# Optimization experiments

Hardware: AMD Instinct MI355X
Metric: run time of the kernel (lower is better)

Reference implementation:

```python
import jax, jax.numpy as jnp
import numpy as np

B, SRC_LEN, IN_DIM = 4096, 128, 16
H = 64
SEQ_LEN = 100
MEAN_DIM = 4
COV_DIM = MEAN_DIM + MEAN_DIM * (MEAN_DIM - 1) // 2  # 10
SKIP = 4


def _lin_init(key, out_d, in_d):
    k1, k2 = jax.random.split(key)
    bound = 1.0 / np.sqrt(in_d)
    W = jax.random.uniform(k1, (out_d, in_d), minval=-bound, maxval=bound, dtype=jnp.float32)
    b = jax.random.uniform(k2, (out_d,), minval=-bound, maxval=bound, dtype=jnp.float32)
    return W, b


def setup_inputs() -> dict:
    key = jax.random.key(0)
    ks = jax.random.split(key, 16)
    inp = {}
    inp["x"] = jax.random.normal(ks[0], (B, SRC_LEN, IN_DIM), dtype=jnp.float32)
    inp["trg"] = jax.random.normal(ks[1], (B, 1, SKIP), dtype=jnp.float32)
    # encoder GRU (1 layer)
    inp["enc_Wih"], inp["enc_bih"] = _lin_init(ks[2], 3 * H, IN_DIM)
    inp["enc_Whh"], inp["enc_bhh"] = _lin_init(ks[3], 3 * H, H)
    # decoder GRU (1 layer)
    inp["dec_Wih"], inp["dec_bih"] = _lin_init(ks[4], 3 * H, IN_DIM)
    inp["dec_Whh"], inp["dec_bhh"] = _lin_init(ks[5], 3 * H, H)
    # decoder.out: Linear(H -> IN_DIM)
    inp["out_W"], inp["out_b"] = _lin_init(ks[6], IN_DIM, H)
    # initEmbed: Linear(SKIP -> IN_DIM)
    inp["emb_W"], inp["emb_b"] = _lin_init(ks[7], IN_DIM, SKIP)
    # mean head: Linear(IN_DIM->H), GELU, Linear(H->MEAN_DIM)
    inp["mh_W1"], inp["mh_b1"] = _lin_init(ks[8], H, IN_DIM)
    inp["mh_W2"], inp["mh_b2"] = _lin_init(ks[9], MEAN_DIM, H)
    # cov head: Linear(IN_DIM->H), GELU, Linear(H->COV_DIM)
    inp["ch_W1"], inp["ch_b1"] = _lin_init(ks[10], H, IN_DIM)
    inp["ch_W2"], inp["ch_b2"] = _lin_init(ks[11], COV_DIM, H)
    return inp


def _gru_cell(h, xt, Wih, Whh, bih, bhh):
    # PyTorch GRU cell math. h, xt: [B, H], [B, in]
    gi = xt @ Wih.T + bih           # [B, 3H]
    gh = h @ Whh.T + bhh            # [B, 3H]
    i_r, i_z, i_n = jnp.split(gi, 3, axis=-1)
    h_r, h_z, h_n = jnp.split(gh, 3, axis=-1)
    r = jax.nn.sigmoid(i_r + h_r)
    z = jax.nn.sigmoid(i_z + h_z)
    n = jnp.tanh(i_n + r * h_n)
    return (1.0 - z) * n + z * h


def reference(x, trg, enc_Wih, enc_bih, enc_Whh, enc_bhh,
              dec_Wih, dec_bih, dec_Whh, dec_bhh,
              out_W, out_b, emb_W, emb_b,
              mh_W1, mh_b1, mh_W2, mh_b2,
              ch_W1, ch_b1, ch_W2, ch_b2):
    b = x.shape[0]
    # ---- encoder GRU over src_len; only final hidden is used downstream ----
    h0 = jnp.zeros((b, H), dtype=x.dtype)

    def enc_step(h, xt):
        h = _gru_cell(h, xt, enc_Wih, enc_Whh, enc_bih, enc_bhh)
        return h, None

    enc_h, _ = jax.lax.scan(enc_step, h0, jnp.swapaxes(x, 0, 1))

    init_in = trg[:, 0, :] @ emb_W.T + emb_b  # [B, IN_DIM]

    def dec_step(carry, _):
        h, inp = carry
        h = _gru_cell(h, inp, dec_Wih, dec_Whh, dec_bih, dec_bhh)
        o = h @ out_W.T + out_b               # [B, IN_DIM]
        nxt = jax.lax.stop_gradient(o)        # .detach() on fed-back input
        return (h, nxt), o

    (_, _), outs = jax.lax.scan(dec_step, (enc_h, init_in), None, length=SEQ_LEN)
    dec_out = jnp.swapaxes(outs, 0, 1)        # [B, SEQ_LEN, IN_DIM]

    # ---- output heads (Dropout is identity in eval) ----
    means = jax.nn.gelu(dec_out @ mh_W1.T + mh_b1, approximate=False) @ mh_W2.T + mh_b2
    covs = jax.nn.gelu(dec_out @ ch_W1.T + ch_b1, approximate=False) @ ch_W2.T + ch_b2

    inf = jnp.inf
    lower = jnp.array([-inf, -inf, -1.0, -1.0], dtype=means.dtype)
    upper = jnp.array([inf, inf, 1.0, 1.0], dtype=means.dtype)
    means = jnp.maximum(jnp.minimum(means, upper), lower)
    return means, covs
```

## Files before the change

kernel.cpp:

```cpp
#include <hip/hip_runtime.h>
#include <cstdint>
#include <cstddef>

#define BTOT    4096
#define SRCLEN  128
#define INDIM   16
#define HDIM    64
#define SEQLEN  100
#define MEANS_N (BTOT * SEQLEN * 4)

__device__ __forceinline__ float sigmoidf_(float x) {
    return __builtin_amdgcn_rcpf(1.0f + __expf(-x));
}
__device__ __forceinline__ float tanhf_(float x) {
    float e = __expf(2.0f * x);
    return 1.0f - 2.0f * __builtin_amdgcn_rcpf(e + 1.0f);
}
__device__ __forceinline__ float gelu_fast(float x) {
    float z = fabsf(x) * 0.70710678118654752440f;
    float t = __builtin_amdgcn_rcpf(1.0f + 0.3275911f * z);
    float p = t * (0.254829592f +
              t * (-0.284496736f +
              t * (1.421413741f +
              t * (-1.453152027f +
              t * 1.061405429f))));
    float er = 1.0f - p * __expf(-z * z);
    er = copysignf(er, x);
    return 0.5f * x * (1.0f + er);
}

typedef __attribute__((ext_vector_type(8))) short s8v;
typedef __attribute__((ext_vector_type(4))) float f4v;

__device__ __forceinline__ unsigned short f2bf(float x) {
    unsigned u = __float_as_uint(x);
    unsigned r = (u + 0x7FFFu + ((u >> 16) & 1u)) >> 16;
    return (unsigned short)r;
}
__device__ __forceinline__ float bf2f(unsigned short b) {
    return __uint_as_float(((unsigned)b) << 16);
}
__device__ __forceinline__ void split2(float4 a, float4 b, s8v& hi, s8v& lo) {
    float v[8] = {a.x, a.y, a.z, a.w, b.x, b.y, b.z, b.w};
    #pragma unroll
    for (int j = 0; j < 8; ++j) {
        unsigned short h = f2bf(v[j]);
        hi[j] = (short)h;
        lo[j] = (short)f2bf(v[j] - bf2f(h));
    }
}
__device__ __forceinline__ void split8(const float* v, s8v& hi, s8v& lo) {
    #pragma unroll
    for (int j = 0; j < 8; ++j) {
        unsigned short h = f2bf(v[j]);
        hi[j] = (short)h;
        lo[j] = (short)f2bf(v[j] - bf2f(h));
    }
}
__device__ __forceinline__ void load_bfrag(const float* p, s8v& hi, s8v& lo) {
    float4 a = *(const float4*)p;
    float4 b = *(const float4*)(p + 4);
    split2(a, b, hi, lo);
}

typedef __attribute__((ext_vector_type(2))) unsigned int u2v;
__device__ __forceinline__ float half_merge(float own_lo, float send_hi) {
    u2v r = __builtin_amdgcn_permlane32_swap(__float_as_uint(own_lo),
                                             __float_as_uint(send_hi),
                                             false, false);
    return __uint_as_float(r[0]);
}

#define MFMA16(a, b, c) __builtin_amdgcn_mfma_f32_16x16x32_bf16((a), (b), (c), 0, 0, 0)

__global__ __launch_bounds__(256, 2) void enc_mfma_kernel(
    const float* __restrict__ x,
    const float* __restrict__ Wih, const float* __restrict__ bih,
    const float* __restrict__ Whh, const float* __restrict__ bhh,
    float* __restrict__ enc_h)
{
    const int tid  = threadIdx.x;
    const int lane = tid & 63;
    const int w    = tid >> 6;
    const int col  = lane & 15;
    const int q    = lane >> 4;
    const int u    = w * 16 + col;
    const int b0   = blockIdx.x * 8;
    const int rj0  = (q & 1) * 4 + ((q >> 1) << 1);

    __shared__ __align__(16) unsigned short hiL[2][16][72];
    __shared__ __align__(16) unsigned short loL[2][16][72];
    __shared__ __align__(16) unsigned short xhi_l[64][9][16];
    __shared__ __align__(16) unsigned short xlo_l[64][9][16];

    for (int i = tid; i < 2 * 16 * 72; i += 256) {
        ((unsigned short*)hiL)[i] = 0;
        ((unsigned short*)loL)[i] = 0;
    }
    for (int i = tid; i < 64 * 16; i += 256) {
        xhi_l[i >> 4][8][i & 15] = 0;
        xlo_l[i >> 4][8][i & 15] = 0;
    }

    auto stage_x = [&](int c) {
        #pragma unroll
        for (int k = 0; k < 8; ++k) {
            int f   = tid + k * 256;
            int b   = f >> 8;
            int rem = f & 255;
            int tl  = rem >> 2;
            int d4  = (rem & 3) << 2;
            const float* xp = x + ((size_t)(b0 + b) * SRCLEN + (c * 64 + tl)) * INDIM + d4;
            float4 v = *(const float4*)xp;
            float vv[4] = {v.x, v.y, v.z, v.w};
            unsigned short hh[4], ll[4];
            #pragma unroll
            for (int j = 0; j < 4; ++j) {
                hh[j] = f2bf(vv[j]);
                ll[j] = f2bf(vv[j] - bf2f(hh[j]));
            }
            *(ushort4*)&xhi_l[tl][b][d4] = make_ushort4(hh[0], hh[1], hh[2], hh[3]);
            *(ushort4*)&xlo_l[tl][b][d4] = make_ushort4(ll[0], ll[1], ll[2], ll[3]);
        }
    };

    const s8v z8 = {0, 0, 0, 0, 0, 0, 0, 0};
    const f4v z4 = {0.0f, 0.0f, 0.0f, 0.0f};

    s8v brh[3], brl[3], bzh[3], bzl[3], bnhh[2], bnhl[2], bnxh, bnxl;
    load_bfrag(Whh + (size_t)u * 64 + q * 8,              brh[0], brl[0]);
    load_bfrag(Whh + (size_t)u * 64 + 32 + q * 8,         brh[1], brl[1]);
    load_bfrag(Whh + (size_t)(64 + u) * 64 + q * 8,       bzh[0], bzl[0]);
    load_bfrag(Whh + (size_t)(64 + u) * 64 + 32 + q * 8,  bzh[1], bzl[1]);
    load_bfrag(Whh + (size_t)(128 + u) * 64 + q * 8,      bnhh[0], bnhl[0]);
    load_bfrag(Whh + (size_t)(128 + u) * 64 + 32 + q * 8, bnhh[1], bnhl[1]);
    if (q < 2) {
        load_bfrag(Wih + (size_t)u * 16 + q * 8,         brh[2], brl[2]);
        load_bfrag(Wih + (size_t)(64 + u) * 16 + q * 8,  bzh[2], bzl[2]);
        load_bfrag(Wih + (size_t)(128 + u) * 16 + q * 8, bnxh, bnxl);
    } else {
        brh[2] = z8; brl[2] = z8; bzh[2] = z8; bzl[2] = z8; bnxh = z8; bnxl = z8;
    }

    const float br   = bih[u] + bhh[u];
    const float bz   = bih[u + 64] + bhh[u + 64];
    const float bnx  = bih[u + 128];
    const float bnh  = bhh[u + 128];

    const int xb   = (q < 2) ? (col & 7) : 8;
    const int xoff = (q & 1) * 8;
    const unsigned short* xh_base = &xhi_l[0][xb][xoff];
    const unsigned short* xl_base = &xlo_l[0][xb][xoff];

    stage_x(0);
    float hold2[2] = {0.0f, 0.0f};
    __syncthreads();

    int cur = 0;
    for (int t = 0; t < SRCLEN; ++t) {
        if (t == 64) {
            stage_x(1);
            __syncthreads();
        }
        const int tl = t & 63;

        const s8v xh = *(const s8v*)(xh_base + (size_t)tl * 144);
        const s8v xl = *(const s8v*)(xl_base + (size_t)tl * 144);

        const s8v ah0 = *(const s8v*)&hiL[cur][col][q * 8];
        const s8v al0 = *(const s8v*)&loL[cur][col][q * 8];
        const s8v ah1 = *(const s8v*)&hiL[cur][col][32 + q * 8];
        const s8v al1 = *(const s8v*)&loL[cur][col][32 + q * 8];

        f4v accr, accz, accnh, accnx;
        accr  = MFMA16(ah0, brh[0], z4);
        accz  = MFMA16(ah0, bzh[0], z4);
        accnh = MFMA16(ah0, bnhh[0], z4);
        accr  = MFMA16(ah0, brl[0], accr);
        accz  = MFMA16(ah0, bzl[0], accz);
        accnh = MFMA16(ah0, bnhl[0], accnh);
        accr  = MFMA16(al0, brh[0], accr);
        accz  = MFMA16(al0, bzh[0], accz);
        accnh = MFMA16(al0, bnhh[0], accnh);
        accr  = MFMA16(ah1, brh[1], accr);
        accz  = MFMA16(ah1, bzh[1], accz);
        accnh = MFMA16(ah1, bnhh[1], accnh);
        accr  = MFMA16(ah1, brl[1], accr);
        accz  = MFMA16(ah1, bzl[1], accz);
        accnh = MFMA16(ah1, bnhl[1], accnh);
        accr  = MFMA16(al1, brh[1], accr);
        accz  = MFMA16(al1, bzh[1], accz);
        accnh = MFMA16(al1, bnhh[1], accnh);
        accr  = MFMA16(xh, brh[2], accr);
        accz  = MFMA16(xh, bzh[2], accz);
        accnx = MFMA16(xh, bnxh, z4);
        accr  = MFMA16(xh, brl[2], accr);
        accz  = MFMA16(xh, bzl[2], accz);
        accnx = MFMA16(xh, bnxl, accnx);
        accr  = MFMA16(xl, brh[2], accr);
        accz  = MFMA16(xl, bzh[2], accz);
        accnx = MFMA16(xl, bnxh, accnx);

        float pr[2], pz[2], pnh[2], pnx[2];
        pr[0]  = half_merge(accr[0],  accr[2]);
        pr[1]  = half_merge(accr[1],  accr[3]);
        pz[0]  = half_merge(accz[0],  accz[2]);
        pz[1]  = half_merge(accz[1],  accz[3]);
        pnh[0] = half_merge(accnh[0], accnh[2]);
        pnh[1] = half_merge(accnh[1], accnh[3]);
        pnx[0] = half_merge(accnx[0], accnx[2]);
        pnx[1] = half_merge(accnx[1], accnx[3]);

        const int nxt = cur ^ 1;
        #pragma unroll
        for (int j = 0; j < 2; ++j) {
            float r  = sigmoidf_(pr[j] + br);
            float zz = sigmoidf_(pz[j] + bz);
            float n  = tanhf_(pnx[j] + bnx + r * (pnh[j] + bnh));
            float h  = (1.0f - zz) * n + zz * hold2[j];
            hold2[j] = h;
            unsigned short hh = f2bf(h);
            hiL[nxt][rj0 + j][u] = hh;
            loL[nxt][rj0 + j][u] = f2bf(h - bf2f(hh));
        }
        __syncthreads();
        cur ^= 1;
    }

    enc_h[(size_t)(b0 + rj0) * HDIM + u]     = hold2[0];
    enc_h[(size_t)(b0 + rj0 + 1) * HDIM + u] = hold2[1];
}

__global__ __launch_bounds__(256, 2) void dec_mfma_kernel(
    const float* __restrict__ trg,
    const float* __restrict__ Wih, const float* __restrict__ bih,
    const float* __restrict__ Whh, const float* __restrict__ bhh,
    const float* __restrict__ outW, const float* __restrict__ outb,
    const float* __restrict__ embW, const float* __restrict__ embb,
    const float* __restrict__ enc_h,
    float* __restrict__ dec_o)
{
    const int tid  = threadIdx.x;
    const int lane = tid & 63;
    const int w    = tid >> 6;
    const int col  = lane & 15;
    const int q    = lane >> 4;
    const int u    = w * 16 + col;
    const int b0   = blockIdx.x * 8;
    const int rj0  = (q & 1) * 4 + ((q >> 1) << 1);

    __shared__ __align__(16) unsigned short hiL[2][16][72];
    __shared__ __align__(16) unsigned short loL[2][16][72];
    __shared__ float outW_l[16][64];
    __shared__ float init_l[8][16];

    for (int i = tid; i < 16 * 64; i += 256) outW_l[i >> 6][i & 63] = outW[i];
    if (tid < 128) {
        int b = tid >> 4, jj = tid & 15;
        float s = embb[jj];
        #pragma unroll
        for (int s4 = 0; s4 < 4; ++s4)
            s = fmaf(embW[jj * 4 + s4], trg[(size_t)(b0 + b) * 4 + s4], s);
        init_l[b][jj] = s;
    }
    for (int i = tid; i < 2 * 8 * 72; i += 256) {
        int buf = i / (8 * 72);
        int rr  = (i / 72) & 7;
        int cc  = i % 72;
        hiL[buf][8 + rr][cc] = 0;
        loL[buf][8 + rr][cc] = 0;
    }
    if (tid < 128) {
        int idx = tid * 4;
        int bb = idx >> 6, uu = idx & 63;
        float4 v = *(const float4*)(enc_h + (size_t)(b0 + bb) * HDIM + uu);
        float vv[4] = {v.x, v.y, v.z, v.w};
        #pragma unroll
        for (int j = 0; j < 4; ++j) {
            unsigned short hh = f2bf(vv[j]);
            hiL[0][bb][uu + j] = hh;
            loL[0][bb][uu + j] = f2bf(vv[j] - bf2f(hh));
        }
    }
    float hold2[2];
    hold2[0] = enc_h[(size_t)(b0 + rj0) * HDIM + u];
    hold2[1] = enc_h[(size_t)(b0 + rj0 + 1) * HDIM + u];

    __syncthreads();

    const f4v z4 = {0.0f, 0.0f, 0.0f, 0.0f};

    float wh_r[16], wh_z[16], wh_n[16];
    #pragma unroll
    for (int c = 0; c < 2; ++c)
        #pragma unroll
        for (int jj = 0; jj < 8; ++jj) {
            int k = c * 32 + q * 8 + jj;
            wh_r[c * 8 + jj] = Whh[(size_t)u * 64 + k];
            wh_z[c * 8 + jj] = Whh[(size_t)(64 + u) * 64 + k];
            wh_n[c * 8 + jj] = Whh[(size_t)(128 + u) * 64 + k];
        }
    float wi_r[16], wi_z[16], wi_n[16];
    #pragma unroll
    for (int j = 0; j < 16; ++j) {
        wi_r[j] = Wih[(size_t)u * 16 + j];
        wi_z[j] = Wih[(size_t)(64 + u) * 16 + j];
        wi_n[j] = Wih[(size_t)(128 + u) * 16 + j];
    }

    float m_r[16], m_z[16], c_in[16];
    #pragma unroll
    for (int c = 0; c < 2; ++c)
        #pragma unroll
        for (int jj = 0; jj < 8; ++jj) {
            int k = c * 32 + q * 8 + jj;
            float sr = 0.0f, sz = 0.0f, sn = 0.0f;
            #pragma unroll
            for (int j = 0; j < 16; ++j) {
                float ow = outW_l[j][k];
                sr = fmaf(wi_r[j], ow, sr);
                sz = fmaf(wi_z[j], ow, sz);
                sn = fmaf(wi_n[j], ow, sn);
            }
            m_r[c * 8 + jj]  = wh_r[c * 8 + jj] + sr;
            m_z[c * 8 + jj]  = wh_z[c * 8 + jj] + sz;
            c_in[c * 8 + jj] = sn;
        }

    s8v mrh[2], mrl[2], mzh[2], mzl[2], cinh[2], cinl[2], hnh[2], hnl[2];
    split8(m_r,      mrh[0],  mrl[0]);  split8(m_r + 8,  mrh[1],  mrl[1]);
    split8(m_z,      mzh[0],  mzl[0]);  split8(m_z + 8,  mzh[1],  mzl[1]);
    split8(c_in,     cinh[0], cinl[0]); split8(c_in + 8, cinh[1], cinl[1]);
    split8(wh_n,     hnh[0],  hnl[0]);  split8(wh_n + 8, hnh[1],  hnl[1]);
    s8v r0h[2], r0l[2], z0h[2], z0l[2];
    split8(wh_r, r0h[0], r0l[0]); split8(wh_r + 8, r0h[1], r0l[1]);
    split8(wh_z, z0h[0], z0l[0]); split8(wh_z + 8, z0h[1], z0l[1]);
    s8v owh[2], owl[2];
    {
        float ov[16];
        #pragma unroll
        for (int c = 0; c < 2; ++c)
            #pragma unroll
            for (int jj = 0; jj < 8; ++jj)
                ov[c * 8 + jj] = outW_l[col][c * 32 + q * 8 + jj];
        split8(ov, owh[0], owl[0]); split8(ov + 8, owh[1], owl[1]);
    }

    float b_r = bhh[u] + bih[u];
    float b_z = bhh[u + 64] + bih[u + 64];
    float b_in = bih[u + 128];
    const float b_hn = bhh[u + 128];
    #pragma unroll
    for (int j = 0; j < 16; ++j) {
        float obj = outb[j];
        b_r  = fmaf(obj, wi_r[j], b_r);
        b_z  = fmaf(obj, wi_z[j], b_z);
        b_in = fmaf(obj, wi_n[j], b_in);
    }
    const float ob = outb[col];

    float g_r[2], g_z[2], g_n[2];
    #pragma unroll
    for (int j2 = 0; j2 < 2; ++j2) {
        int row = rj0 + j2;
        float sr = bih[u] + bhh[u];
        float sz = bih[u + 64] + bhh[u + 64];
        float sn = bih[u + 128];
        #pragma unroll
        for (int j = 0; j < 16; ++j) {
            float iv = init_l[row][j];
            sr = fmaf(wi_r[j], iv, sr);
            sz = fmaf(wi_z[j], iv, sz);
            sn = fmaf(wi_n[j], iv, sn);
        }
        g_r[j2] = sr; g_z[j2] = sz; g_n[j2] = sn;
    }

    {
        const s8v ah0 = *(const s8v*)&hiL[0][col][q * 8];
        const s8v al0 = *(const s8v*)&loL[0][col][q * 8];
        const s8v ah1 = *(const s8v*)&hiL[0][col][32 + q * 8];
        const s8v al1 = *(const s8v*)&loL[0][col][32 + q * 8];
        f4v ar, az, ahn;
        ar  = MFMA16(ah0, r0h[0], z4);
        az  = MFMA16(ah0, z0h[0], z4);
        ahn = MFMA16(ah0, hnh[0], z4);
        ar  = MFMA16(ah0, r0l[0], ar);
        az  = MFMA16(ah0, z0l[0], az);
        ahn = MFMA16(ah0, hnl[0], ahn);
        ar  = MFMA16(al0, r0h[0], ar);
        az  = MFMA16(al0, z0h[0], az);
        ahn = MFMA16(al0, hnh[0], ahn);
        ar  = MFMA16(ah1, r0h[1], ar);
        az  = MFMA16(ah1, z0h[1], az);
        ahn = MFMA16(ah1, hnh[1], ahn);
        ar  = MFMA16(ah1, r0l[1], ar);
        az  = MFMA16(ah1, z0l[1], az);
        ahn = MFMA16(ah1, hnl[1], ahn);
        ar  = MFMA16(al1, r0h[1], ar);
        az  = MFMA16(al1, z0h[1], az);
        ahn = MFMA16(al1, hnh[1], ahn);

        float pr[2], pz[2], pnh[2];
        pr[0]  = half_merge(ar[0],  ar[2]);
        pr[1]  = half_merge(ar[1],  ar[3]);
        pz[0]  = half_merge(az[0],  az[2]);
        pz[1]  = half_merge(az[1],  az[3]);
        pnh[0] = half_merge(ahn[0], ahn[2]);
        pnh[1] = half_merge(ahn[1], ahn[3]);

        #pragma unroll
        for (int j = 0; j < 2; ++j) {
            float r  = sigmoidf_(pr[j] + g_r[j]);
            float zz = sigmoidf_(pz[j] + g_z[j]);
            float n  = tanhf_(g_n[j] + r * (pnh[j] + b_hn));
            float h  = (1.0f - zz) * n + zz * hold2[j];
            hold2[j] = h;
            unsigned short hh = f2bf(h);
            hiL[1][rj0 + j][u] = hh;
            loL[1][rj0 + j][u] = f2bf(h - bf2f(hh));
        }
        __syncthreads();
    }

    for (int t = 1; t < SEQLEN; ++t) {
        const int cur = t & 1;
        const s8v ah0 = *(const s8v*)&hiL[cur][col][q * 8];
        const s8v al0 = *(const s8v*)&loL[cur][col][q * 8];
        const s8v ah1 = *(const s8v*)&hiL[cur][col][32 + q * 8];
        const s8v al1 = *(const s8v*)&loL[cur][col][32 + q * 8];

        if (w == ((t - 1) & 3)) {
            f4v oa;
            oa = MFMA16(ah0, owh[0], z4);
            oa = MFMA16(ah0, owl[0], oa);
            oa = MFMA16(al0, owh[0], oa);
            oa = MFMA16(ah1, owh[1], oa);
            oa = MFMA16(ah1, owl[1], oa);
            oa = MFMA16(al1, owh[1], oa);
            if (q < 2) {
                #pragma unroll
                for (int i = 0; i < 4; ++i)
                    dec_o[(((size_t)(b0 + q * 4 + i) * SEQLEN) + (t - 1)) * INDIM + col] = oa[i] + ob;
            }
        }

        f4v ar, az, ain, ahn;
        ar  = MFMA16(ah0, mrh[0], z4);
        az  = MFMA16(ah0, mzh[0], z4);
        ain = MFMA16(ah0, cinh[0], z4);
        ahn = MFMA16(ah0, hnh[0], z4);
        ar  = MFMA16(ah0, mrl[0], ar);
        az  = MFMA16(ah0, mzl[0], az);
        ain = MFMA16(ah0, cinl[0], ain);
        ahn = MFMA16(ah0, hnl[0], ahn);
        ar  = MFMA16(al0, mrh[0], ar);
        az  = MFMA16(al0, mzh[0], az);
        ain = MFMA16(al0, cinh[0], ain);
        ahn = MFMA16(al0, hnh[0], ahn);
        ar  = MFMA16(ah1, mrh[1], ar);
        az  = MFMA16(ah1, mzh[1], az);
        ain = MFMA16(ah1, cinh[1], ain);
        ahn = MFMA16(ah1, hnh[1], ahn);
        ar  = MFMA16(ah1, mrl[1], ar);
        az  = MFMA16(ah1, mzl[1], az);
        ain = MFMA16(ah1, cinl[1], ain);
        ahn = MFMA16(ah1, hnl[1], ahn);
        ar  = MFMA16(al1, mrh[1], ar);
        az  = MFMA16(al1, mzh[1], az);
        ain = MFMA16(al1, cinh[1], ain);
        ahn = MFMA16(al1, hnh[1], ahn);

        float pr[2], pz[2], pin[2], pnh[2];
        pr[0]  = half_merge(ar[0],  ar[2]);
        pr[1]  = half_merge(ar[1],  ar[3]);
        pz[0]  = half_merge(az[0],  az[2]);
        pz[1]  = half_merge(az[1],  az[3]);
        pin[0] = half_merge(ain[0], ain[2]);
        pin[1] = half_merge(ain[1], ain[3]);
        pnh[0] = half_merge(ahn[0], ahn[2]);
        pnh[1] = half_merge(ahn[1], ahn[3]);

        const int nxt = cur ^ 1;
        #pragma unroll
        for (int j = 0; j < 2; ++j) {
            float r  = sigmoidf_(pr[j] + b_r);
            float zz = sigmoidf_(pz[j] + b_z);
            float n  = tanhf_(pin[j] + b_in + r * (pnh[j] + b_hn));
            float h  = (1.0f - zz) * n + zz * hold2[j];
            hold2[j] = h;
            unsigned short hh = f2bf(h);
            hiL[nxt][rj0 + j][u] = hh;
            loL[nxt][rj0 + j][u] = f2bf(h - bf2f(hh));
        }
        __syncthreads();
    }

    if (w == 0) {
        const s8v ah0 = *(const s8v*)&hiL[0][col][q * 8];
        const s8v al0 = *(const s8v*)&loL[0][col][q * 8];
        const s8v ah1 = *(const s8v*)&hiL[0][col][32 + q * 8];
        const s8v al1 = *(const s8v*)&loL[0][col][32 + q * 8];
        f4v oa;
        oa = MFMA16(ah0, owh[0], z4);
        oa = MFMA16(ah0, owl[0], oa);
        oa = MFMA16(al0, owh[0], oa);
        oa = MFMA16(ah1, owh[1], oa);
        oa = MFMA16(ah1, owl[1], oa);
        oa = MFMA16(al1, owh[1], oa);
        if (q < 2) {
            #pragma unroll
            for (int i = 0; i < 4; ++i)
                dec_o[(((size_t)(b0 + q * 4 + i) * SEQLEN) + (SEQLEN - 1)) * INDIM + col] = oa[i] + ob;
        }
    }
}

__global__ __launch_bounds__(256) void heads_kernel(
    const float* __restrict__ dec_o,
    const float* __restrict__ mW1, const float* __restrict__ mb1,
    const float* __restrict__ mW2, const float* __restrict__ mb2,
    const float* __restrict__ cW1, const float* __restrict__ cb1,
    const float* __restrict__ cW2, const float* __restrict__ cb2,
    float* __restrict__ out)
{
    const int tid = threadIdx.x;

    __shared__ __align__(16) float lW1m[64][16];
    __shared__ __align__(16) float lW1c[64][16];
    __shared__ __align__(16) float lW2t[64][16];

    for (int i = tid; i < 1024; i += 256) {
        lW1m[i >> 4][i & 15] = mW1[i];
        lW1c[i >> 4][i & 15] = cW1[i];
    }
    if (tid < 64) {
        #pragma unroll
        for (int j = 0; j < 4; ++j)  lW2t[tid][j]     = mW2[j * 64 + tid];
        #pragma unroll
        for (int j = 0; j < 10; ++j) lW2t[tid][4 + j] = cW2[j * 64 + tid];
        lW2t[tid][14] = mb1[tid];
        lW2t[tid][15] = cb1[tid];
    }
    __syncthreads();

    const size_t r = (size_t)blockIdx.x * 256 + tid;

    float o16[16];
    {
        const float4* op = (const float4*)(dec_o + r * 16);
        #pragma unroll
        for (int c = 0; c < 4; ++c) {
            float4 v = op[c];
            o16[4 * c + 0] = v.x; o16[4 * c + 1] = v.y;
            o16[4 * c + 2] = v.z; o16[4 * c + 3] = v.w;
        }
    }

    float m[4], cv[10];
    #pragma unroll
    for (int j = 0; j < 4; ++j)  m[j]  = mb2[j];
    #pragma unroll
    for (int j = 0; j < 10; ++j) cv[j] = cb2[j];

    #pragma unroll 4
    for (int hu = 0; hu < 64; ++hu) {
        const float4 a0 = *(const float4*)&lW1m[hu][0];
        const float4 a1 = *(const float4*)&lW1m[hu][4];
        const float4 a2 = *(const float4*)&lW1m[hu][8];
        const float4 a3 = *(const float4*)&lW1m[hu][12];
        const float4 c0 = *(const float4*)&lW1c[hu][0];
        const float4 c1 = *(const float4*)&lW1c[hu][4];
        const float4 c2 = *(const float4*)&lW1c[hu][8];
        const float4 c3 = *(const float4*)&lW1c[hu][12];
        const float4 t0 = *(const float4*)&lW2t[hu][0];
        const float4 t1 = *(const float4*)&lW2t[hu][4];
        const float4 t2 = *(const float4*)&lW2t[hu][8];
        const float4 t3 = *(const float4*)&lW2t[hu][12];

        float hm = t3.z;
        hm = fmaf(a0.x, o16[0],  hm); hm = fmaf(a0.y, o16[1],  hm);
        hm = fmaf(a0.z, o16[2],  hm); hm = fmaf(a0.w, o16[3],  hm);
        hm = fmaf(a1.x, o16[4],  hm); hm = fmaf(a1.y, o16[5],  hm);
        hm = fmaf(a1.z, o16[6],  hm); hm = fmaf(a1.w, o16[7],  hm);
        hm = fmaf(a2.x, o16[8],  hm); hm = fmaf(a2.y, o16[9],  hm);
        hm = fmaf(a2.z, o16[10], hm); hm = fmaf(a2.w, o16[11], hm);
        hm = fmaf(a3.x, o16[12], hm); hm = fmaf(a3.y, o16[13], hm);
        hm = fmaf(a3.z, o16[14], hm); hm = fmaf(a3.w, o16[15], hm);
        float gm = gelu_fast(hm);
        m[0] = fmaf(t0.x, gm, m[0]); m[1] = fmaf(t0.y, gm, m[1]);
        m[2] = fmaf(t0.z, gm, m[2]); m[3] = fmaf(t0.w, gm, m[3]);

        float hc = t3.w;
        hc = fmaf(c0.x, o16[0],  hc); hc = fmaf(c0.y, o16[1],  hc);
        hc = fmaf(c0.z, o16[2],  hc); hc = fmaf(c0.w, o16[3],  hc);
        hc = fmaf(c1.x, o16[4],  hc); hc = fmaf(c1.y, o16[5],  hc);
        hc = fmaf(c1.z, o16[6],  hc); hc = fmaf(c1.w, o16[7],  hc);
        hc = fmaf(c2.x, o16[8],  hc); hc = fmaf(c2.y, o16[9],  hc);
        hc = fmaf(c2.z, o16[10], hc); hc = fmaf(c2.w, o16[11], hc);
        hc = fmaf(c3.x, o16[12], hc); hc = fmaf(c3.y, o16[13], hc);
        hc = fmaf(c3.z, o16[14], hc); hc = fmaf(c3.w, o16[15], hc);
        float gc = gelu_fast(hc);
        cv[0] = fmaf(t1.x, gc, cv[0]); cv[1] = fmaf(t1.y, gc, cv[1]);
        cv[2] = fmaf(t1.z, gc, cv[2]); cv[3] = fmaf(t1.w, gc, cv[3]);
        cv[4] = fmaf(t2.x, gc, cv[4]); cv[5] = fmaf(t2.y, gc, cv[5]);
        cv[6] = fmaf(t2.z, gc, cv[6]); cv[7] = fmaf(t2.w, gc, cv[7]);
        cv[8] = fmaf(t3.x, gc, cv[8]); cv[9] = fmaf(t3.y, gc, cv[9]);
    }

    m[2] = fminf(fmaxf(m[2], -1.0f), 1.0f);
    m[3] = fminf(fmaxf(m[3], -1.0f), 1.0f);

    float* means = out;
    float* covs  = out + MEANS_N;
    #pragma unroll
    for (int j = 0; j < 4; ++j)  means[r * 4 + j]  = m[j];
    #pragma unroll
    for (int j = 0; j < 10; ++j) covs[r * 10 + j]  = cv[j];
}

extern "C" void kernel_launch(void* const* d_in, const int* in_sizes, int n_in,
                              void* d_out, int out_size, void* d_ws, size_t ws_size,
                              hipStream_t stream)
{
    const float* x    = (const float*)d_in[0];
    const float* trg  = (const float*)d_in[1];
    const float* eWih = (const float*)d_in[2];
    const float* ebih = (const float*)d_in[3];
    const float* eWhh = (const float*)d_in[4];
    const float* ebhh = (const float*)d_in[5];
    const float* dWih = (const float*)d_in[6];
    const float* dbih = (const float*)d_in[7];
    const float* dWhh = (const float*)d_in[8];
    const float* dbhh = (const float*)d_in[9];
    const float* outW = (const float*)d_in[10];
    const float* outb = (const float*)d_in[11];
    const float* embW = (const float*)d_in[12];
    const float* embb = (const float*)d_in[13];
    const float* mW1  = (const float*)d_in[14];
    const float* mb1  = (const float*)d_in[15];
    const float* mW2  = (const float*)d_in[16];
    const float* mb2  = (const float*)d_in[17];
    const float* cW1  = (const float*)d_in[18];
    const float* cb1  = (const float*)d_in[19];
    const float* cW2  = (const float*)d_in[20];
    const float* cb2  = (const float*)d_in[21];

    float* ws    = (float*)d_ws;
    float* enc_h = ws;
    float* dec_o = ws + (size_t)BTOT * HDIM;
    float* outp  = (float*)d_out;

    enc_mfma_kernel<<<dim3(BTOT / 8), dim3(256), 0, stream>>>(x, eWih, ebih, eWhh, ebhh, enc_h);
    dec_mfma_kernel<<<dim3(BTOT / 8), dim3(256), 0, stream>>>(trg, dWih, dbih, dWhh, dbhh,
                                                              outW, outb, embW, embb, enc_h, dec_o);
    heads_kernel<<<dim3((BTOT * SEQLEN) / 256), dim3(256), 0, stream>>>(
        dec_o, mW1, mb1, mW2, mb2, cW1, cb1, cW2, cb2, outp);
}
```

Before: 347.9 us.

## Split encoder GRU gates across two wave groups with 16 batches per block

The encoder kernel now uses 512 threads and 16 batch rows per block, filling the full 16-row MFMA tile instead of half of it. Four waves compute the r gate and the recurrent n term, and the other four compute the z gate and the input n term, exchanging partial results through shared memory. The aim is to halve the blocks and MFMA work per batch row and to shorten each wave's serial MFMA chain per time step. The cost is an extra __syncthreads per step, an LDS round trip for the exchanged gates, and more frequent x staging in 32-step chunks.

```diff
diff --git a/kernel.cpp b/kernel.cpp
--- a/kernel.cpp
+++ b/kernel.cpp
@@ -73,7 +73,7 @@
 
 #define MFMA16(a, b, c) __builtin_amdgcn_mfma_f32_16x16x32_bf16((a), (b), (c), 0, 0, 0)
 
-__global__ __launch_bounds__(256, 2) void enc_mfma_kernel(
+__global__ __launch_bounds__(512, 2) void enc_mfma_kernel(
     const float* __restrict__ x,
     const float* __restrict__ Wih, const float* __restrict__ bih,
     const float* __restrict__ Whh, const float* __restrict__ bhh,
@@ -82,35 +82,37 @@
     const int tid  = threadIdx.x;
     const int lane = tid & 63;
     const int w    = tid >> 6;
+    const int p    = w & 3;
+    const bool isA = (w < 4);
     const int col  = lane & 15;
     const int q    = lane >> 4;
-    const int u    = w * 16 + col;
-    const int b0   = blockIdx.x * 8;
-    const int rj0  = (q & 1) * 4 + ((q >> 1) << 1);
+    const int u    = p * 16 + col;
+    const int b0   = blockIdx.x * 16;
 
     __shared__ __align__(16) unsigned short hiL[2][16][72];
     __shared__ __align__(16) unsigned short loL[2][16][72];
-    __shared__ __align__(16) unsigned short xhi_l[64][9][16];
-    __shared__ __align__(16) unsigned short xlo_l[64][9][16];
-
-    for (int i = tid; i < 2 * 16 * 72; i += 256) {
+    __shared__ __align__(16) unsigned short xhi_l[32][17][16];
+    __shared__ __align__(16) unsigned short xlo_l[32][17][16];
+    __shared__ float zx_l[4][8][64];
+
+    for (int i = tid; i < 2 * 16 * 72; i += 512) {
         ((unsigned short*)hiL)[i] = 0;
         ((unsigned short*)loL)[i] = 0;
     }
-    for (int i = tid; i < 64 * 16; i += 256) {
-        xhi_l[i >> 4][8][i & 15] = 0;
-        xlo_l[i >> 4][8][i & 15] = 0;
+    for (int i = tid; i < 32 * 16; i += 512) {
+        xhi_l[i >> 4][16][i & 15] = 0;
+        xlo_l[i >> 4][16][i & 15] = 0;
     }
 
     auto stage_x = [&](int c) {
         #pragma unroll
-        for (int k = 0; k < 8; ++k) {
-            int f   = tid + k * 256;
-            int b   = f >> 8;
-            int rem = f & 255;
+        for (int k = 0; k < 4; ++k) {
+            int f   = tid + k * 512;
+            int b   = f >> 7;
+            int rem = f & 127;
             int tl  = rem >> 2;
             int d4  = (rem & 3) << 2;
-            const float* xp = x + ((size_t)(b0 + b) * SRCLEN + (c * 64 + tl)) * INDIM + d4;
+            const float* xp = x + ((size_t)(b0 + b) * SRCLEN + (c * 32 + tl)) * INDIM + d4;
             float4 v = *(const float4*)xp;
             float vv[4] = {v.x, v.y, v.z, v.w};
             unsigned short hh[4], ll[4];
@@ -127,108 +129,107 @@
     const s8v z8 = {0, 0, 0, 0, 0, 0, 0, 0};
     const f4v z4 = {0.0f, 0.0f, 0.0f, 0.0f};
 
-    s8v brh[3], brl[3], bzh[3], bzl[3], bnhh[2], bnhl[2], bnxh, bnxl;
-    load_bfrag(Whh + (size_t)u * 64 + q * 8,              brh[0], brl[0]);
-    load_bfrag(Whh + (size_t)u * 64 + 32 + q * 8,         brh[1], brl[1]);
-    load_bfrag(Whh + (size_t)(64 + u) * 64 + q * 8,       bzh[0], bzl[0]);
-    load_bfrag(Whh + (size_t)(64 + u) * 64 + 32 + q * 8,  bzh[1], bzl[1]);
-    load_bfrag(Whh + (size_t)(128 + u) * 64 + q * 8,      bnhh[0], bnhl[0]);
-    load_bfrag(Whh + (size_t)(128 + u) * 64 + 32 + q * 8, bnhh[1], bnhl[1]);
-    if (q < 2) {
-        load_bfrag(Wih + (size_t)u * 16 + q * 8,         brh[2], brl[2]);
-        load_bfrag(Wih + (size_t)(64 + u) * 16 + q * 8,  bzh[2], bzl[2]);
-        load_bfrag(Wih + (size_t)(128 + u) * 16 + q * 8, bnxh, bnxl);
+    const int g1row = (isA ? 0 : 64) + u;
+    s8v g1h[3], g1l[3];
+    s8v g2h[2], g2l[2];
+    load_bfrag(Whh + (size_t)g1row * 64 + q * 8,      g1h[0], g1l[0]);
+    load_bfrag(Whh + (size_t)g1row * 64 + 32 + q * 8, g1h[1], g1l[1]);
+    if (q < 2) load_bfrag(Wih + (size_t)g1row * 16 + q * 8, g1h[2], g1l[2]);
+    else { g1h[2] = z8; g1l[2] = z8; }
+    if (isA) {
+        load_bfrag(Whh + (size_t)(128 + u) * 64 + q * 8,      g2h[0], g2l[0]);
+        load_bfrag(Whh + (size_t)(128 + u) * 64 + 32 + q * 8, g2h[1], g2l[1]);
     } else {
-        brh[2] = z8; brl[2] = z8; bzh[2] = z8; bzl[2] = z8; bnxh = z8; bnxl = z8;
-    }
-
-    const float br   = bih[u] + bhh[u];
-    const float bz   = bih[u + 64] + bhh[u + 64];
-    const float bnx  = bih[u + 128];
-    const float bnh  = bhh[u + 128];
-
-    const int xb   = (q < 2) ? (col & 7) : 8;
+        if (q < 2) load_bfrag(Wih + (size_t)(128 + u) * 16 + q * 8, g2h[0], g2l[0]);
+        else { g2h[0] = z8; g2l[0] = z8; }
+        g2h[1] = z8; g2l[1] = z8;
+    }
+
+    const float br  = bih[u] + bhh[u];
+    const float bz  = bih[u + 64] + bhh[u + 64];
+    const float bnx = bih[u + 128];
+    const float bnh = bhh[u + 128];
+
+    const int xb   = (q < 2) ? col : 16;
     const int xoff = (q & 1) * 8;
     const unsigned short* xh_base = &xhi_l[0][xb][xoff];
     const unsigned short* xl_base = &xlo_l[0][xb][xoff];
 
     stage_x(0);
-    float hold2[2] = {0.0f, 0.0f};
+    float hold4[4] = {0.0f, 0.0f, 0.0f, 0.0f};
     __syncthreads();
 
     int cur = 0;
     for (int t = 0; t < SRCLEN; ++t) {
-        if (t == 64) {
-            stage_x(1);
+        const int tl = t & 31;
+        if (t && tl == 0) {
+            stage_x(t >> 5);
             __syncthreads();
         }
-        const int tl = t & 63;
-
-        const s8v xh = *(const s8v*)(xh_base + (size_t)tl * 144);
-        const s8v xl = *(const s8v*)(xl_base + (size_t)tl * 144);
+
+        const s8v xh = *(const s8v*)(xh_base + (size_t)tl * 272);
+        const s8v xl = *(const s8v*)(xl_base + (size_t)tl * 272);
 
         const s8v ah0 = *(const s8v*)&hiL[cur][col][q * 8];
         const s8v al0 = *(const s8v*)&loL[cur][col][q * 8];
         const s8v ah1 = *(const s8v*)&hiL[cur][col][32 + q * 8];
         const s8v al1 = *(const s8v*)&loL[cur][col][32 + q * 8];
 
-        f4v accr, accz, accnh, accnx;
-        accr  = MFMA16(ah0, brh[0], z4);
-        accz  = MFMA16(ah0, bzh[0], z4);
-        accnh = MFMA16(ah0, bnhh[0], z4);
-        accr  = MFMA16(ah0, brl[0], accr);
-        accz  = MFMA16(ah0, bzl[0], accz);
-        accnh = MFMA16(ah0, bnhl[0], accnh);
-        accr  = MFMA16(al0, brh[0], accr);
-        accz  = MFMA16(al0, bzh[0], accz);
-        accnh = MFMA16(al0, bnhh[0], accnh);
-        accr  = MFMA16(ah1, brh[1], accr);
-        accz  = MFMA16(ah1, bzh[1], accz);
-        accnh = MFMA16(ah1, bnhh[1], accnh);
-        accr  = MFMA16(ah1, brl[1], accr);
-        accz  = MFMA16(ah1, bzl[1], accz);
-        accnh = MFMA16(ah1, bnhl[1], accnh);
-        accr  = MFMA16(al1, brh[1], accr);
-        accz  = MFMA16(al1, bzh[1], accz);
-        accnh = MFMA16(al1, bnhh[1], accnh);
-        accr  = MFMA16(xh, brh[2], accr);
-        accz  = MFMA16(xh, bzh[2], accz);
-        accnx = MFMA16(xh, bnxh, z4);
-        accr  = MFMA16(xh, brl[2], accr);
-        accz  = MFMA16(xh, bzl[2], accz);
-        accnx = MFMA16(xh, bnxl, accnx);
-        accr  = MFMA16(xl, brh[2], accr);
-        accz  = MFMA16(xl, bzh[2], accz);
-        accnx = MFMA16(xl, bnxh, accnx);
-
-        float pr[2], pz[2], pnh[2], pnx[2];
-        pr[0]  = half_merge(accr[0],  accr[2]);
-        pr[1]  = half_merge(accr[1],  accr[3]);
-        pz[0]  = half_merge(accz[0],  accz[2]);
-        pz[1]  = half_merge(accz[1],  accz[3]);
-        pnh[0] = half_merge(accnh[0], accnh[2]);
-        pnh[1] = half_merge(accnh[1], accnh[3]);
-        pnx[0] = half_merge(accnx[0], accnx[2]);
-        pnx[1] = half_merge(accnx[1], accnx[3]);
-
-        const int nxt = cur ^ 1;
-        #pragma unroll
-        for (int j = 0; j < 2; ++j) {
-            float r  = sigmoidf_(pr[j] + br);
-            float zz = sigmoidf_(pz[j] + bz);
-            float n  = tanhf_(pnx[j] + bnx + r * (pnh[j] + bnh));
-            float h  = (1.0f - zz) * n + zz * hold2[j];
-            hold2[j] = h;
-            unsigned short hh = f2bf(h);
-            hiL[nxt][rj0 + j][u] = hh;
-            loL[nxt][rj0 + j][u] = f2bf(h - bf2f(hh));
+        f4v a1;
+        a1 = MFMA16(ah0, g1h[0], z4);
+        a1 = MFMA16(ah0, g1l[0], a1);
+        a1 = MFMA16(al0, g1h[0], a1);
+        a1 = MFMA16(ah1, g1h[1], a1);
+        a1 = MFMA16(ah1, g1l[1], a1);
+        a1 = MFMA16(al1, g1h[1], a1);
+        a1 = MFMA16(xh,  g1h[2], a1);
+        a1 = MFMA16(xh,  g1l[2], a1);
+        a1 = MFMA16(xl,  g1h[2], a1);
+
+        f4v a2;
+        if (isA) {
+            a2 = MFMA16(ah0, g2h[0], z4);
+            a2 = MFMA16(ah0, g2l[0], a2);
+            a2 = MFMA16(al0, g2h[0], a2);
+            a2 = MFMA16(ah1, g2h[1], a2);
+            a2 = MFMA16(ah1, g2l[1], a2);
+            a2 = MFMA16(al1, g2h[1], a2);
+        } else {
+            a2 = MFMA16(xh, g2h[0], z4);
+            a2 = MFMA16(xh, g2l[0], a2);
+            a2 = MFMA16(xl, g2h[0], a2);
+            #pragma unroll
+            for (int i = 0; i < 4; ++i) {
+                zx_l[p][i][lane]     = a1[i];
+                zx_l[p][4 + i][lane] = a2[i];
+            }
+        }
+        __syncthreads();
+
+        if (isA) {
+            const int nxt = cur ^ 1;
+            #pragma unroll
+            for (int i = 0; i < 4; ++i) {
+                float zz = sigmoidf_(zx_l[p][i][lane] + bz);
+                float nx = zx_l[p][4 + i][lane] + bnx;
+                float r  = sigmoidf_(a1[i] + br);
+                float n  = tanhf_(nx + r * (a2[i] + bnh));
+                float h  = (1.0f - zz) * n + zz * hold4[i];
+                hold4[i] = h;
+                unsigned short hh = f2bf(h);
+                hiL[nxt][q * 4 + i][u] = hh;
+                loL[nxt][q * 4 + i][u] = f2bf(h - bf2f(hh));
+            }
         }
         __syncthreads();
         cur ^= 1;
     }
 
-    enc_h[(size_t)(b0 + rj0) * HDIM + u]     = hold2[0];
-    enc_h[(size_t)(b0 + rj0 + 1) * HDIM + u] = hold2[1];
+    if (isA) {
+        #pragma unroll
+        for (int i = 0; i < 4; ++i)
+            enc_h[(size_t)(b0 + q * 4 + i) * HDIM + u] = hold4[i];
+    }
 }
 
 __global__ __launch_bounds__(256, 2) void dec_mfma_kernel(
@@ -651,7 +652,7 @@
     float* dec_o = ws + (size_t)BTOT * HDIM;
     float* outp  = (float*)d_out;
 
-    enc_mfma_kernel<<<dim3(BTOT / 8), dim3(256), 0, stream>>>(x, eWih, ebih, eWhh, ebhh, enc_h);
+    enc_mfma_kernel<<<dim3(BTOT / 16), dim3(512), 0, stream>>>(x, eWih, ebih, eWhh, ebhh, enc_h);
     dec_mfma_kernel<<<dim3(BTOT / 8), dim3(256), 0, stream>>>(trg, dWih, dbih, dWhh, dbhh,
                                                               outW, outb, embW, embb, enc_h, dec_o);
     heads_kernel<<<dim3((BTOT * SEQLEN) / 256), dim3(256), 0, stream>>>(
```

Result: slower. 363.3 us (+4.4%).
